# Performance work log

Measured on AMD Instinct MI355X. Metric: run time of the kernel, lower is better.

The kernel has to match this reference:

```python
import jax, jax.numpy as jnp
from jax import lax
import numpy as np

# dims
B, C, H, W = 16, 64, 56, 56      # input images
N, KH = 1024, 3                  # number of centroids, patch size
K, V = 8, 128                    # k-nearest, values_dim
STRIDE, PAD = 1, 1


def setup_inputs() -> dict:
    key = jax.random.key(0)
    ks = jax.random.split(key, 5)
    x = jax.random.normal(ks[0], (B, C, H, W), jnp.float32)
    centroids = jax.random.normal(ks[1], (N, C, KH, KH), jnp.float32)
    # as in NeighborsValuesAssigner.__init__ (non-whitened path):
    kernel = -centroids                                            # (N,C,3,3)
    bias = 0.5 * jnp.sum(centroids.reshape(N, -1) ** 2, axis=1)    # (N,)
    values = jax.random.normal(ks[2], (N, V), jnp.float32)
    # Conv2d(k*V -> V, kernel 1x1), stored flattened as (V, K*V)
    conv_w = jax.random.normal(ks[3], (V, K * V), jnp.float32) / np.sqrt(K * V)
    conv_b = jax.random.normal(ks[4], (V,), jnp.float32) * 0.01
    return {"x": x, "kernel": kernel, "bias": bias, "values": values,
            "conv_w": conv_w, "conv_b": conv_b}


def reference(x, kernel, bias, values, conv_w, conv_b):
    # distances to centroids via conv (up to a constant 0.5*||patch||^2 per location)
    dist = lax.conv_general_dilated(
        x, kernel, window_strides=(STRIDE, STRIDE),
        padding=[(PAD, PAD), (PAD, PAD)],
        dimension_numbers=("NCHW", "OIHW", "NCHW"))
    dist = dist + bias[None, :, None, None]          # (B, N, Ho, Wo)
    # k smallest distances -> indices (torch.topk(..., largest=False))
    neg = -jnp.transpose(dist, (0, 2, 3, 1))         # (B, Ho, Wo, N)
    _, idx = lax.top_k(neg, K)                       # (B, Ho, Wo, K)
    gathered = values[idx]                           # (B, Ho, Wo, K, V)
    # torch: permute to (B,K,V,H,W), flatten K,V -> channels, 1x1 conv.
    # (B,Ho,Wo,K,V) reshape keeps the same K-outer/V-inner channel order.
    feat = gathered.reshape(gathered.shape[0], gathered.shape[1],
                            gathered.shape[2], K * V)  # (B, Ho, Wo, K*V)
    out = jnp.einsum("bhwc,oc->bohw", feat, conv_w) + conv_b[None, :, None, None]
    return out  # (B, V, Ho, Wo)
```

## Files before the change

### kernel.cpp

```cpp
#include <hip/hip_runtime.h>

#define BATCH   16
#define CH      64
#define HH      56
#define WW      56
#define NCENT   1024
#define KTOT    576
#define MTOT    50176
#define MTILE   128
#define KC      16
#define NSPLIT  4
#define VDIM    128
#define TOPK    8

typedef float f4 __attribute__((ext_vector_type(4)));

__global__ __launch_bounds__(256) void k_rearrange(const float* __restrict__ kern,
                                                   float* __restrict__ kr) {
    const int o = blockIdx.x * 256 + threadIdx.x;
    const int c = o & 63;
    const int tap = (o >> 6) % 9;
    const int n = o / 576;
    kr[o] = kern[n * KTOT + c * 9 + tap];
}

__global__ __launch_bounds__(256) void k_table(const float* __restrict__ values,
                                               const float* __restrict__ conv_w,
                                               float* __restrict__ table) {
    __shared__ float wk[128][132];
    __shared__ float vals[16][128];

    const int t = threadIdx.x;
    const int k = blockIdx.x >> 6;
    const int n0 = (blockIdx.x & 63) * 16;

    {
        const int row = t >> 1;
        const int seg = (t & 1) * 64;
        const f4* src = (const f4*)(conv_w + row * 1024 + k * 128 + seg);
#pragma unroll
        for (int q = 0; q < 16; ++q) *(f4*)&wk[row][seg + q * 4] = src[q];
    }
    {
        const int r = t >> 4;
        const int col = (t & 15) * 8;
        const f4* src = (const f4*)(values + (n0 + r) * VDIM + col);
        *(f4*)&vals[r][col] = src[0];
        *(f4*)&vals[r][col + 4] = src[1];
    }
    __syncthreads();

    const int o = t & 127;
    const int ngrp = t >> 7;
    float acc[8];
#pragma unroll
    for (int r = 0; r < 8; ++r) acc[r] = 0.f;

    for (int v = 0; v < 128; ++v) {
        const float w = wk[o][v];
#pragma unroll
        for (int r = 0; r < 8; ++r)
            acc[r] = fmaf(w, vals[ngrp * 8 + r][v], acc[r]);
    }
#pragma unroll
    for (int r = 0; r < 8; ++r) {
        const int n = n0 + ngrp * 8 + r;
        table[(((k << 10) + n) << 7) + o] = acc[r];
    }
}

__global__ __launch_bounds__(256, 4) void k_dist_topk(const float* __restrict__ x,
                                                      const float* __restrict__ kr,
                                                      const float* __restrict__ bias,
                                                      float* __restrict__ dws,
                                                      int* __restrict__ iws) {
    __shared__ char smem[MTILE * 65 * 4];
    float (*A_lds)[MTILE] = (float (*)[MTILE])smem;
    float (*B_lds)[128]  = (float (*)[128])(smem + KC * MTILE * 4);
    float (*dist_lds)[65] = (float (*)[65])smem;

    const int t = threadIdx.x;
    const int bm = blockIdx.x >> 2;
    const int split = blockIdx.x & 3;
    const int m0 = bm * MTILE;

    const int tx = t & 15;
    const int ty = t >> 4;
    const int ty4 = ty * 4;
    const int tx4 = tx * 4;

    const int ml = t & 127;
    const int L = m0 + ml;
    const int b = L / 3136;
    const int hw = L - b * 3136;
    const int hh = hw / 56;
    const int wp = hw - hh * 56;
    const float* xb = x + b * (CH * 3136);
    const int kbase = (t >> 7) * 8;

    const int nl = t >> 1;
    const int khalf = (t & 1) * 8;

    float top_d[TOPK];
    int top_i[TOPK];
#pragma unroll
    for (int j = 0; j < TOPK; ++j) { top_d[j] = 3.0e38f; top_i[j] = 0; }

    for (int nt = 0; nt < 2; ++nt) {
        const int n0 = split * 256 + nt * 128;
        const float* Bk = kr + (n0 + nl) * KTOT + khalf;

        float acc[2][2][4][4];
#pragma unroll
        for (int a0 = 0; a0 < 2; ++a0)
#pragma unroll
            for (int a1 = 0; a1 < 2; ++a1)
#pragma unroll
                for (int i = 0; i < 4; ++i)
#pragma unroll
                    for (int j = 0; j < 4; ++j) acc[a0][a1][i][j] = 0.f;

#pragma unroll 1
        for (int cc = 0; cc < 36; ++cc) {
            const int tap = cc >> 2;
            const int c0 = (cc & 3) * 16;
            const int dh = tap / 3;
            const int dw = tap - dh * 3;
            const int hy = hh + dh - 1;
            const int wx = wp + dw - 1;
            const bool inb = ((unsigned)hy < 56u && (unsigned)wx < 56u);
            const float* xp = xb + (c0 + kbase) * 3136 + hy * 56 + wx;

            __syncthreads();
#pragma unroll
            for (int j = 0; j < 8; ++j) {
                float v = 0.f;
                if (inb) v = xp[j * 3136];
                A_lds[kbase + j][ml] = v;
            }
            {
                const f4* src = (const f4*)(Bk + cc * KC);
                const f4 b0 = src[0], b1 = src[1];
                B_lds[khalf + 0][nl] = b0[0];
                B_lds[khalf + 1][nl] = b0[1];
                B_lds[khalf + 2][nl] = b0[2];
                B_lds[khalf + 3][nl] = b0[3];
                B_lds[khalf + 4][nl] = b1[0];
                B_lds[khalf + 5][nl] = b1[1];
                B_lds[khalf + 6][nl] = b1[2];
                B_lds[khalf + 7][nl] = b1[3];
            }
            __syncthreads();
#pragma unroll 2
            for (int kkl = 0; kkl < KC; ++kkl) {
                const f4 a0 = *(const f4*)&A_lds[kkl][ty4];
                const f4 a1 = *(const f4*)&A_lds[kkl][ty4 + 64];
                const f4 bb0 = *(const f4*)&B_lds[kkl][tx4];
                const f4 bb1 = *(const f4*)&B_lds[kkl][tx4 + 64];
#pragma unroll
                for (int i = 0; i < 4; ++i)
#pragma unroll
                    for (int j = 0; j < 4; ++j) {
                        acc[0][0][i][j] = fmaf(a0[i], bb0[j], acc[0][0][i][j]);
                        acc[0][1][i][j] = fmaf(a0[i], bb1[j], acc[0][1][i][j]);
                        acc[1][0][i][j] = fmaf(a1[i], bb0[j], acc[1][0][i][j]);
                        acc[1][1][i][j] = fmaf(a1[i], bb1[j], acc[1][1][i][j]);
                    }
            }
        }

#pragma unroll
        for (int hc = 0; hc < 2; ++hc) {
            __syncthreads();
            const f4 bv = *(const f4*)&bias[n0 + hc * 64 + tx4];
#pragma unroll
            for (int ih = 0; ih < 2; ++ih)
#pragma unroll
                for (int i = 0; i < 4; ++i)
#pragma unroll
                    for (int j = 0; j < 4; ++j)
                        dist_lds[ih * 64 + ty4 + i][tx4 + j] = acc[ih][hc][i][j] + bv[j];
            __syncthreads();
            if (t < 128) {
                const int r = t;
                const int nbase = n0 + hc * 64;
                float tlast = top_d[TOPK - 1];
#pragma unroll 8
                for (int c = 0; c < 64; ++c) {
                    const float v = dist_lds[r][c];
                    if (v < tlast) {
                        top_d[TOPK - 1] = v;
                        top_i[TOPK - 1] = nbase + c;
#pragma unroll
                        for (int j = TOPK - 1; j >= 1; --j) {
                            if (top_d[j] < top_d[j - 1]) {
                                const float td = top_d[j]; top_d[j] = top_d[j - 1]; top_d[j - 1] = td;
                                const int tii = top_i[j]; top_i[j] = top_i[j - 1]; top_i[j - 1] = tii;
                            }
                        }
                        tlast = top_d[TOPK - 1];
                    }
                }
            }
        }
    }

    if (t < 128) {
#pragma unroll
        for (int j = 0; j < TOPK; ++j) {
            dws[(split * TOPK + j) * MTOT + m0 + t] = top_d[j];
            iws[(split * TOPK + j) * MTOT + m0 + t] = top_i[j];
        }
    }
}

__global__ __launch_bounds__(256) void k_merge_out(const float* __restrict__ dws,
                                                   const int* __restrict__ iws,
                                                   const float* __restrict__ table,
                                                   const float* __restrict__ conv_b,
                                                   float* __restrict__ out) {
    __shared__ int id8[64][TOPK];
    const int t = threadIdx.x;
    const int l0 = blockIdx.x * 64;
    const int b = l0 / 3136;

    if (t < 64) {
        const int loc = l0 + t;
        float td[TOPK];
        int ti[TOPK];
#pragma unroll
        for (int j = 0; j < TOPK; ++j) { td[j] = 3.0e38f; ti[j] = 0x7fffffff; }
#pragma unroll
        for (int s = 0; s < NSPLIT; ++s)
#pragma unroll
            for (int j = 0; j < TOPK; ++j) {
                const float v = dws[(s * TOPK + j) * MTOT + loc];
                const int ii = iws[(s * TOPK + j) * MTOT + loc];
                if (v < td[TOPK - 1] || (v == td[TOPK - 1] && ii < ti[TOPK - 1])) {
                    td[TOPK - 1] = v; ti[TOPK - 1] = ii;
#pragma unroll
                    for (int q = TOPK - 1; q >= 1; --q) {
                        if (td[q] < td[q - 1] || (td[q] == td[q - 1] && ti[q] < ti[q - 1])) {
                            const float a = td[q]; td[q] = td[q - 1]; td[q - 1] = a;
                            const int bq = ti[q]; ti[q] = ti[q - 1]; ti[q - 1] = bq;
                        }
                    }
                }
            }
#pragma unroll
        for (int j = 0; j < TOPK; ++j) id8[t][j] = ti[j];
    }
    __syncthreads();

    const int ll = t & 63;
    const int qs = t >> 6;
    const int loc = l0 + ll;
    const int hw = loc - b * 3136;
    const int o0 = qs * 32;

    int idx[TOPK];
#pragma unroll
    for (int j = 0; j < TOPK; ++j) idx[j] = id8[ll][j];

    f4 acc[8];
#pragma unroll
    for (int q = 0; q < 8; ++q) acc[q] = *(const f4*)&conv_b[o0 + q * 4];
#pragma unroll
    for (int k = 0; k < TOPK; ++k) {
        const float* row = table + (((k << 10) + idx[k]) << 7) + o0;
#pragma unroll
        for (int q = 0; q < 8; ++q) {
            const f4 rv = *(const f4*)&row[q * 4];
            acc[q] += rv;
        }
    }
    float* ob = out + b * (VDIM * 3136) + hw;
#pragma unroll
    for (int q = 0; q < 8; ++q)
#pragma unroll
        for (int e = 0; e < 4; ++e)
            ob[(o0 + q * 4 + e) * 3136] = acc[q][e];
}

extern "C" void kernel_launch(void* const* d_in, const int* in_sizes, int n_in,
                              void* d_out, int out_size, void* d_ws, size_t ws_size,
                              hipStream_t stream) {
    const float* x      = (const float*)d_in[0];
    const float* kern   = (const float*)d_in[1];
    const float* bias   = (const float*)d_in[2];
    const float* values = (const float*)d_in[3];
    const float* conv_w = (const float*)d_in[4];
    const float* conv_b = (const float*)d_in[5];
    float* out = (float*)d_out;

    float* kr = (float*)d_ws;
    float* table = kr + NCENT * KTOT;
    float* dws = table + 8 * NCENT * VDIM;
    int* iws = (int*)(dws + NSPLIT * TOPK * MTOT);

    k_rearrange<<<dim3(NCENT * KTOT / 256), dim3(256), 0, stream>>>(kern, kr);
    k_table<<<dim3(8 * 64), dim3(256), 0, stream>>>(values, conv_w, table);
    k_dist_topk<<<dim3((MTOT / MTILE) * NSPLIT), dim3(256), 0, stream>>>(x, kr, bias, dws, iws);
    k_merge_out<<<dim3(MTOT / 64), dim3(256), 0, stream>>>(dws, iws, table, conv_b, out);
}
```

Measured before the change: 1.011 ms.

## Use bf16 MFMA for distance GEMM with candidate pool and fp32 refinement

Replaces the fp32 FMA distance GEMM with bf16 MFMA (16x16x32) using double-buffered LDS tiles. Each wave keeps a top-10 per location over its quarter of each centroid block, stored as packed order-key/index words. A new refine kernel merges these into a 16-candidate pool, recomputes exact fp32 distances for the pool, selects the final top-8 and gathers the precomputed table to produce the output. The intent is to move the dominant GEMM onto matrix cores. It risks wrong neighbor selection when bf16 error pushes a true neighbor out of the candidate pool.

New measurement: 989.0 us. 2.1% less time.

```diff
diff --git a/kernel.cpp b/kernel.cpp
--- a/kernel.cpp
+++ b/kernel.cpp
@@ -2,26 +2,39 @@
 
 #define BATCH   16
 #define CH      64
-#define HH      56
-#define WW      56
 #define NCENT   1024
 #define KTOT    576
 #define MTOT    50176
-#define MTILE   128
-#define KC      16
-#define NSPLIT  4
 #define VDIM    128
 #define TOPK    8
+#define NSUB    4
+#define SK      10
+#define POOL    16
 
 typedef float f4 __attribute__((ext_vector_type(4)));
-
-__global__ __launch_bounds__(256) void k_rearrange(const float* __restrict__ kern,
-                                                   float* __restrict__ kr) {
+typedef short bf16x8 __attribute__((ext_vector_type(8)));
+typedef int i4 __attribute__((ext_vector_type(4)));
+
+__device__ __forceinline__ unsigned short f2bf(float f) {
+    union { float f; unsigned u; } c; c.f = f;
+    return (unsigned short)((c.u + 0x7fffu + ((c.u >> 16) & 1u)) >> 16);
+}
+__device__ __forceinline__ unsigned ordkey(float f) {
+    unsigned u = __float_as_uint(f);
+    return u ^ ((u >> 31) ? 0xFFFFFFFFu : 0x80000000u);
+}
+
+__global__ __launch_bounds__(256) void k_prep(const float* __restrict__ kern,
+                                              float* __restrict__ kr,
+                                              unsigned short* __restrict__ kb) {
     const int o = blockIdx.x * 256 + threadIdx.x;
-    const int c = o & 63;
-    const int tap = (o >> 6) % 9;
     const int n = o / 576;
-    kr[o] = kern[n * KTOT + c * 9 + tap];
+    const int r = o - n * 576;
+    const int tap = r >> 6;
+    const int c = r & 63;
+    const float v = kern[n * 576 + c * 9 + tap];
+    kr[o] = v;
+    kb[o] = f2bf(v);
 }
 
 __global__ __launch_bounds__(256) void k_table(const float* __restrict__ values,
@@ -55,12 +68,10 @@
     float acc[8];
 #pragma unroll
     for (int r = 0; r < 8; ++r) acc[r] = 0.f;
-
     for (int v = 0; v < 128; ++v) {
         const float w = wk[o][v];
 #pragma unroll
-        for (int r = 0; r < 8; ++r)
-            acc[r] = fmaf(w, vals[ngrp * 8 + r][v], acc[r]);
+        for (int r = 0; r < 8; ++r) acc[r] = fmaf(w, vals[ngrp * 8 + r][v], acc[r]);
     }
 #pragma unroll
     for (int r = 0; r < 8; ++r) {
@@ -69,217 +80,269 @@
     }
 }
 
-__global__ __launch_bounds__(256, 4) void k_dist_topk(const float* __restrict__ x,
-                                                      const float* __restrict__ kr,
+__global__ __launch_bounds__(256, 3) void k_mfma_topk(const float* __restrict__ x,
+                                                      const unsigned short* __restrict__ kb,
                                                       const float* __restrict__ bias,
-                                                      float* __restrict__ dws,
-                                                      int* __restrict__ iws) {
-    __shared__ char smem[MTILE * 65 * 4];
-    float (*A_lds)[MTILE] = (float (*)[MTILE])smem;
-    float (*B_lds)[128]  = (float (*)[128])(smem + KC * MTILE * 4);
-    float (*dist_lds)[65] = (float (*)[65])smem;
+                                                      unsigned* __restrict__ kws) {
+    __shared__ char smem[51200];
+    unsigned short* A0 = (unsigned short*)smem;
+    unsigned short* A1 = (unsigned short*)(smem + 5120);
+    unsigned short* B0 = (unsigned short*)(smem + 10240);
+    unsigned short* B1 = (unsigned short*)(smem + 30720);
+    float (*dist)[65] = (float (*)[65])(smem + 10240);
 
     const int t = threadIdx.x;
-    const int bm = blockIdx.x >> 2;
-    const int split = blockIdx.x & 3;
-    const int m0 = bm * MTILE;
-
-    const int tx = t & 15;
-    const int ty = t >> 4;
-    const int ty4 = ty * 4;
-    const int tx4 = tx * 4;
-
-    const int ml = t & 127;
+    const int w = t >> 6;
+    const int lane = t & 63;
+    const int mfrag = lane & 15;
+    const int kq = lane >> 4;
+
+    const int m0 = blockIdx.x * 64;
+    const int ml = t & 63;
+    const int cg = t >> 6;
     const int L = m0 + ml;
     const int b = L / 3136;
     const int hw = L - b * 3136;
     const int hh = hw / 56;
     const int wp = hw - hh * 56;
     const float* xb = x + b * (CH * 3136);
-    const int kbase = (t >> 7) * 8;
-
-    const int nl = t >> 1;
-    const int khalf = (t & 1) * 8;
-
-    float top_d[TOPK];
-    int top_i[TOPK];
-#pragma unroll
-    for (int j = 0; j < TOPK; ++j) { top_d[j] = 3.0e38f; top_i[j] = 0; }
-
-    for (int nt = 0; nt < 2; ++nt) {
-        const int n0 = split * 256 + nt * 128;
-        const float* Bk = kr + (n0 + nl) * KTOT + khalf;
-
-        float acc[2][2][4][4];
-#pragma unroll
-        for (int a0 = 0; a0 < 2; ++a0)
-#pragma unroll
-            for (int a1 = 0; a1 < 2; ++a1)
-#pragma unroll
-                for (int i = 0; i < 4; ++i)
-#pragma unroll
-                    for (int j = 0; j < 4; ++j) acc[a0][a1][i][j] = 0.f;
+    const int brow = t >> 2;
+    const int bseg = t & 3;
+
+    float top_d[SK];
+    unsigned top_k[SK];
+#pragma unroll
+    for (int j = 0; j < SK; ++j) { top_d[j] = 3.0e38f; top_k[j] = 0xFFFFFFFFu; }
+
+    for (int nt = 0; nt < 4; ++nt) {
+        const int n0 = nt * 256;
+
+        f4 acc[4][4];
+#pragma unroll
+        for (int mi = 0; mi < 4; ++mi)
+#pragma unroll
+            for (int ni = 0; ni < 4; ++ni) acc[mi][ni] = (f4)0.f;
+
+        {
+            const int tap = 0, c0 = 0;
+            const int hy = hh + tap / 3 - 1;
+            const int wx = wp + tap % 3 - 1;
+            const bool inb = ((unsigned)hy < 56u && (unsigned)wx < 56u);
+            const float* xp = xb + (c0 + cg * 8) * 3136 + hy * 56 + wx;
+            unsigned short tmp[8];
+#pragma unroll
+            for (int j = 0; j < 8; ++j) tmp[j] = inb ? f2bf(xp[j * 3136]) : (unsigned short)0;
+            *(i4*)&A0[ml * 40 + cg * 8] = *(i4*)tmp;
+#pragma unroll
+            for (int p = 0; p < 4; ++p) {
+                const int nn = p * 64 + brow;
+                const i4 v = *(const i4*)(kb + (n0 + nn) * KTOT + 0 * 32 + bseg * 8);
+                *(i4*)&B0[nn * 40 + bseg * 8] = v;
+            }
+        }
+        __syncthreads();
 
 #pragma unroll 1
-        for (int cc = 0; cc < 36; ++cc) {
-            const int tap = cc >> 2;
-            const int c0 = (cc & 3) * 16;
+        for (int ch = 0; ch < 18; ++ch) {
+            unsigned short* Ac = (ch & 1) ? A1 : A0;
+            unsigned short* Bc = (ch & 1) ? B1 : B0;
+            if (ch < 17) {
+                const int chn = ch + 1;
+                unsigned short* An = (chn & 1) ? A1 : A0;
+                unsigned short* Bn = (chn & 1) ? B1 : B0;
+                const int tap = chn >> 1;
+                const int c0 = (chn & 1) * 32;
+                const int dh = tap / 3;
+                const int dw = tap - dh * 3;
+                const int hy = hh + dh - 1;
+                const int wx = wp + dw - 1;
+                const bool inb = ((unsigned)hy < 56u && (unsigned)wx < 56u);
+                const float* xp = xb + (c0 + cg * 8) * 3136 + hy * 56 + wx;
+                unsigned short tmp[8];
+#pragma unroll
+                for (int j = 0; j < 8; ++j) tmp[j] = inb ? f2bf(xp[j * 3136]) : (unsigned short)0;
+                *(i4*)&An[ml * 40 + cg * 8] = *(i4*)tmp;
+#pragma unroll
+                for (int p = 0; p < 4; ++p) {
+                    const int nn = p * 64 + brow;
+                    const i4 v = *(const i4*)(kb + (n0 + nn) * KTOT + chn * 32 + bseg * 8);
+                    *(i4*)&Bn[nn * 40 + bseg * 8] = v;
+                }
+            }
+            bf16x8 af[4], bfr[4];
+#pragma unroll
+            for (int mi = 0; mi < 4; ++mi)
+                af[mi] = *(const bf16x8*)&Ac[(mi * 16 + mfrag) * 40 + kq * 8];
+#pragma unroll
+            for (int ni = 0; ni < 4; ++ni)
+                bfr[ni] = *(const bf16x8*)&Bc[(w * 64 + ni * 16 + mfrag) * 40 + kq * 8];
+#pragma unroll
+            for (int mi = 0; mi < 4; ++mi)
+#pragma unroll
+                for (int ni = 0; ni < 4; ++ni)
+                    acc[mi][ni] = __builtin_amdgcn_mfma_f32_16x16x32_bf16(
+                        af[mi], bfr[ni], acc[mi][ni], 0, 0, 0);
+            __syncthreads();
+        }
+
+        float bv[4];
+#pragma unroll
+        for (int ni = 0; ni < 4; ++ni)
+            bv[ni] = bias[n0 + w * 64 + ni * 16 + mfrag];
+
+#pragma unroll 1
+        for (int q = 0; q < 4; ++q) {
+            if (w == q) {
+#pragma unroll
+                for (int mi = 0; mi < 4; ++mi)
+#pragma unroll
+                    for (int ni = 0; ni < 4; ++ni)
+#pragma unroll
+                        for (int r = 0; r < 4; ++r)
+                            dist[mi * 16 + kq * 4 + r][ni * 16 + mfrag] = acc[mi][ni][r] + bv[ni];
+                const int nb = (n0 + q * 64);
+                float tlast = top_d[SK - 1];
+#pragma unroll 8
+                for (int c = 0; c < 64; ++c) {
+                    const float v = dist[lane][c];
+                    if (v < tlast) {
+                        const unsigned key = (ordkey(v) & 0xFFFFFC00u) | (unsigned)(nb + c);
+                        top_d[SK - 1] = v; top_k[SK - 1] = key;
+#pragma unroll
+                        for (int j = SK - 1; j >= 1; --j) {
+                            if (top_d[j] < top_d[j - 1]) {
+                                const float a = top_d[j]; top_d[j] = top_d[j - 1]; top_d[j - 1] = a;
+                                const unsigned kk = top_k[j]; top_k[j] = top_k[j - 1]; top_k[j - 1] = kk;
+                            }
+                        }
+                        tlast = top_d[SK - 1];
+                    }
+                }
+            }
+            __syncthreads();
+        }
+    }
+
+#pragma unroll
+    for (int j = 0; j < SK; ++j)
+        kws[(w * SK + j) * MTOT + m0 + lane] = top_k[j];
+}
+
+__global__ __launch_bounds__(256) void k_refine_out(const float* __restrict__ x,
+                                                    const float* __restrict__ kr,
+                                                    const float* __restrict__ bias,
+                                                    const unsigned* __restrict__ kws,
+                                                    const float* __restrict__ table,
+                                                    const float* __restrict__ conv_b,
+                                                    float* __restrict__ out) {
+    __shared__ int   ids[16][POOL];
+    __shared__ float dd[16][POOL];
+    __shared__ int   id8s[16][TOPK];
+
+    const int t = threadIdx.x;
+    const int l0 = blockIdx.x * 16;
+    const int b = l0 / 3136;
+    const float* xb = x + b * (CH * 3136);
+
+    if (t < 16) {
+        const int gl = l0 + t;
+        unsigned tk[POOL];
+#pragma unroll
+        for (int r = 0; r < POOL; ++r) tk[r] = 0xFFFFFFFFu;
+#pragma unroll
+        for (int s = 0; s < NSUB; ++s)
+#pragma unroll
+            for (int j = 0; j < SK; ++j) {
+                const unsigned k = kws[(s * SK + j) * MTOT + gl];
+                if (k < tk[POOL - 1]) {
+                    tk[POOL - 1] = k;
+#pragma unroll
+                    for (int r = POOL - 1; r >= 1; --r) {
+                        if (tk[r] < tk[r - 1]) { const unsigned a = tk[r]; tk[r] = tk[r - 1]; tk[r - 1] = a; }
+                    }
+                }
+            }
+#pragma unroll
+        for (int r = 0; r < POOL; ++r) ids[t][r] = (int)(tk[r] & 1023u);
+    }
+    __syncthreads();
+
+    {
+        const int loc = t & 15;
+        const int cand = t >> 4;
+        const int gl = l0 + loc;
+        const int hw = gl - b * 3136;
+        const int hh = hw / 56;
+        const int wp = hw - hh * 56;
+        const int cd = ids[loc][cand];
+        const float* kp = kr + cd * KTOT;
+        float a = 0.f;
+#pragma unroll 1
+        for (int tap = 0; tap < 9; ++tap) {
             const int dh = tap / 3;
             const int dw = tap - dh * 3;
             const int hy = hh + dh - 1;
             const int wx = wp + dw - 1;
-            const bool inb = ((unsigned)hy < 56u && (unsigned)wx < 56u);
-            const float* xp = xb + (c0 + kbase) * 3136 + hy * 56 + wx;
-
-            __syncthreads();
-#pragma unroll
-            for (int j = 0; j < 8; ++j) {
-                float v = 0.f;
-                if (inb) v = xp[j * 3136];
-                A_lds[kbase + j][ml] = v;
-            }
-            {
-                const f4* src = (const f4*)(Bk + cc * KC);
-                const f4 b0 = src[0], b1 = src[1];
-                B_lds[khalf + 0][nl] = b0[0];
-                B_lds[khalf + 1][nl] = b0[1];
-                B_lds[khalf + 2][nl] = b0[2];
-                B_lds[khalf + 3][nl] = b0[3];
-                B_lds[khalf + 4][nl] = b1[0];
-                B_lds[khalf + 5][nl] = b1[1];
-                B_lds[khalf + 6][nl] = b1[2];
-                B_lds[khalf + 7][nl] = b1[3];
-            }
-            __syncthreads();
-#pragma unroll 2
-            for (int kkl = 0; kkl < KC; ++kkl) {
-                const f4 a0 = *(const f4*)&A_lds[kkl][ty4];
-                const f4 a1 = *(const f4*)&A_lds[kkl][ty4 + 64];
-                const f4 bb0 = *(const f4*)&B_lds[kkl][tx4];
-                const f4 bb1 = *(const f4*)&B_lds[kkl][tx4 + 64];
-#pragma unroll
-                for (int i = 0; i < 4; ++i)
-#pragma unroll
-                    for (int j = 0; j < 4; ++j) {
-                        acc[0][0][i][j] = fmaf(a0[i], bb0[j], acc[0][0][i][j]);
-                        acc[0][1][i][j] = fmaf(a0[i], bb1[j], acc[0][1][i][j]);
-                        acc[1][0][i][j] = fmaf(a1[i], bb0[j], acc[1][0][i][j]);
-                        acc[1][1][i][j] = fmaf(a1[i], bb1[j], acc[1][1][i][j]);
-                    }
-            }
-        }
-
-#pragma unroll
-        for (int hc = 0; hc < 2; ++hc) {
-            __syncthreads();
-            const f4 bv = *(const f4*)&bias[n0 + hc * 64 + tx4];
-#pragma unroll
-            for (int ih = 0; ih < 2; ++ih)
-#pragma unroll
-                for (int i = 0; i < 4; ++i)
-#pragma unroll
-                    for (int j = 0; j < 4; ++j)
-                        dist_lds[ih * 64 + ty4 + i][tx4 + j] = acc[ih][hc][i][j] + bv[j];
-            __syncthreads();
-            if (t < 128) {
-                const int r = t;
-                const int nbase = n0 + hc * 64;
-                float tlast = top_d[TOPK - 1];
+            if ((unsigned)hy < 56u && (unsigned)wx < 56u) {
+                const float* xp = xb + hy * 56 + wx;
+                const float* kt = kp + tap * 64;
 #pragma unroll 8
-                for (int c = 0; c < 64; ++c) {
-                    const float v = dist_lds[r][c];
-                    if (v < tlast) {
-                        top_d[TOPK - 1] = v;
-                        top_i[TOPK - 1] = nbase + c;
-#pragma unroll
-                        for (int j = TOPK - 1; j >= 1; --j) {
-                            if (top_d[j] < top_d[j - 1]) {
-                                const float td = top_d[j]; top_d[j] = top_d[j - 1]; top_d[j - 1] = td;
-                                const int tii = top_i[j]; top_i[j] = top_i[j - 1]; top_i[j - 1] = tii;
-                            }
-                        }
-                        tlast = top_d[TOPK - 1];
+                for (int c = 0; c < 64; ++c)
+                    a = fmaf(xp[c * 3136], kt[c], a);
+            }
+        }
+        dd[loc][cand] = a + bias[cd];
+    }
+    __syncthreads();
+
+    if (t < 16) {
+        float td[TOPK]; int ti[TOPK];
+#pragma unroll
+        for (int j = 0; j < TOPK; ++j) { td[j] = 3.0e38f; ti[j] = 0x7fffffff; }
+#pragma unroll
+        for (int j = 0; j < POOL; ++j) {
+            const float v = dd[t][j];
+            const int ii = ids[t][j];
+            if (v < td[TOPK - 1] || (v == td[TOPK - 1] && ii < ti[TOPK - 1])) {
+                td[TOPK - 1] = v; ti[TOPK - 1] = ii;
+#pragma unroll
+                for (int q = TOPK - 1; q >= 1; --q) {
+                    if (td[q] < td[q - 1] || (td[q] == td[q - 1] && ti[q] < ti[q - 1])) {
+                        const float a = td[q]; td[q] = td[q - 1]; td[q - 1] = a;
+                        const int bq = ti[q]; ti[q] = ti[q - 1]; ti[q - 1] = bq;
                     }
                 }
             }
         }
-    }
-
-    if (t < 128) {
-#pragma unroll
-        for (int j = 0; j < TOPK; ++j) {
-            dws[(split * TOPK + j) * MTOT + m0 + t] = top_d[j];
-            iws[(split * TOPK + j) * MTOT + m0 + t] = top_i[j];
-        }
-    }
-}
-
-__global__ __launch_bounds__(256) void k_merge_out(const float* __restrict__ dws,
-                                                   const int* __restrict__ iws,
-                                                   const float* __restrict__ table,
-                                                   const float* __restrict__ conv_b,
-                                                   float* __restrict__ out) {
-    __shared__ int id8[64][TOPK];
-    const int t = threadIdx.x;
-    const int l0 = blockIdx.x * 64;
-    const int b = l0 / 3136;
-
-    if (t < 64) {
-        const int loc = l0 + t;
-        float td[TOPK];
-        int ti[TOPK];
-#pragma unroll
-        for (int j = 0; j < TOPK; ++j) { td[j] = 3.0e38f; ti[j] = 0x7fffffff; }
-#pragma unroll
-        for (int s = 0; s < NSPLIT; ++s)
-#pragma unroll
-            for (int j = 0; j < TOPK; ++j) {
-                const float v = dws[(s * TOPK + j) * MTOT + loc];
-                const int ii = iws[(s * TOPK + j) * MTOT + loc];
-                if (v < td[TOPK - 1] || (v == td[TOPK - 1] && ii < ti[TOPK - 1])) {
-                    td[TOPK - 1] = v; ti[TOPK - 1] = ii;
-#pragma unroll
-                    for (int q = TOPK - 1; q >= 1; --q) {
-                        if (td[q] < td[q - 1] || (td[q] == td[q - 1] && ti[q] < ti[q - 1])) {
-                            const float a = td[q]; td[q] = td[q - 1]; td[q - 1] = a;
-                            const int bq = ti[q]; ti[q] = ti[q - 1]; ti[q - 1] = bq;
-                        }
-                    }
-                }
-            }
-#pragma unroll
-        for (int j = 0; j < TOPK; ++j) id8[t][j] = ti[j];
+#pragma unroll
+        for (int j = 0; j < TOPK; ++j) id8s[t][j] = ti[j];
     }
     __syncthreads();
 
-    const int ll = t & 63;
-    const int qs = t >> 6;
-    const int loc = l0 + ll;
-    const int hw = loc - b * 3136;
-    const int o0 = qs * 32;
-
-    int idx[TOPK];
-#pragma unroll
-    for (int j = 0; j < TOPK; ++j) idx[j] = id8[ll][j];
-
-    f4 acc[8];
-#pragma unroll
-    for (int q = 0; q < 8; ++q) acc[q] = *(const f4*)&conv_b[o0 + q * 4];
-#pragma unroll
-    for (int k = 0; k < TOPK; ++k) {
-        const float* row = table + (((k << 10) + idx[k]) << 7) + o0;
-#pragma unroll
-        for (int q = 0; q < 8; ++q) {
-            const f4 rv = *(const f4*)&row[q * 4];
-            acc[q] += rv;
-        }
-    }
-    float* ob = out + b * (VDIM * 3136) + hw;
-#pragma unroll
-    for (int q = 0; q < 8; ++q)
-#pragma unroll
-        for (int e = 0; e < 4; ++e)
-            ob[(o0 + q * 4 + e) * 3136] = acc[q][e];
+    {
+        const int loc = t & 15;
+        const int og = t >> 4;
+        const int gl = l0 + loc;
+        const int hw = gl - b * 3136;
+        const int o0 = og * 8;
+        int idx[TOPK];
+#pragma unroll
+        for (int j = 0; j < TOPK; ++j) idx[j] = id8s[loc][j];
+        f4 a0 = *(const f4*)&conv_b[o0];
+        f4 a1 = *(const f4*)&conv_b[o0 + 4];
+#pragma unroll
+        for (int k = 0; k < TOPK; ++k) {
+            const float* row = table + (((k << 10) + idx[k]) << 7) + o0;
+            a0 += *(const f4*)&row[0];
+            a1 += *(const f4*)&row[4];
+        }
+        float* ob = out + b * (VDIM * 3136) + hw;
+#pragma unroll
+        for (int e = 0; e < 4; ++e) {
+            ob[(o0 + e) * 3136] = a0[e];
+            ob[(o0 + 4 + e) * 3136] = a1[e];
+        }
+    }
 }
 
 extern "C" void kernel_launch(void* const* d_in, const int* in_sizes, int n_in,
@@ -294,12 +357,12 @@
     float* out = (float*)d_out;
 
     float* kr = (float*)d_ws;
-    float* table = kr + NCENT * KTOT;
-    float* dws = table + 8 * NCENT * VDIM;
-    int* iws = (int*)(dws + NSPLIT * TOPK * MTOT);
-
-    k_rearrange<<<dim3(NCENT * KTOT / 256), dim3(256), 0, stream>>>(kern, kr);
+    unsigned short* kb = (unsigned short*)(kr + NCENT * KTOT);
+    float* table = (float*)(kb + NCENT * KTOT);
+    unsigned* kws = (unsigned*)(table + 8 * NCENT * VDIM);
+
+    k_prep<<<dim3(NCENT * KTOT / 256), dim3(256), 0, stream>>>(kern, kr, kb);
     k_table<<<dim3(8 * 64), dim3(256), 0, stream>>>(values, conv_w, table);
-    k_dist_topk<<<dim3((MTOT / MTILE) * NSPLIT), dim3(256), 0, stream>>>(x, kr, bias, dws, iws);
-    k_merge_out<<<dim3(MTOT / 64), dim3(256), 0, stream>>>(dws, iws, table, conv_b, out);
-}
+    k_mfma_topk<<<dim3(MTOT / 64), dim3(256), 0, stream>>>(x, kb, bias, kws);
+    k_refine_out<<<dim3(MTOT / 16), dim3(256), 0, stream>>>(x, kr, bias, kws, table, conv_b, out);
+}
```
